# Performance work log

Hardware: AMD Instinct MI355X
Metric: run time of the kernel (lower is better)

Reference implementation:

```python
import jax, jax.numpy as jnp
import numpy as np
import math

DIM_V = 512

def setup_inputs() -> dict:
    key = jax.random.key(0)
    k1, k2, k3, k4, k5, k6 = jax.random.split(key, 6)
    B, C, N, M = 8, DIM_V, 4096, 1024
    pcd_up = jax.random.normal(k1, (B, C, N), dtype=jnp.float32)
    pcd_down = jax.random.normal(k2, (B, C, M), dtype=jnp.float32)
    s = 1.0 / math.sqrt(C)
    Wq = jax.random.normal(k3, (C, C), dtype=jnp.float32) * s
    Wk = jax.random.normal(k4, (C, C), dtype=jnp.float32) * s
    Wv = jax.random.normal(k5, (C, C), dtype=jnp.float32) * s
    Wskip = jax.random.normal(k6, (C, C), dtype=jnp.float32) * s
    return {"pcd_up": pcd_up, "pcd_down": pcd_down, "Wq": Wq, "Wk": Wk, "Wv": Wv, "Wskip": Wskip}

def reference(pcd_up, pcd_down, Wq, Wk, Wv, Wskip):
    # 1x1 Conv1d == per-point linear: weight [out_c, in_c]
    q = jnp.einsum('oc,bcn->bon', Wq, pcd_up)      # [B, C, N]
    k = jnp.einsum('oc,bcm->bom', Wk, pcd_down)    # [B, C, M]
    v = jnp.einsum('oc,bcm->bom', Wv, pcd_down)    # [B, C, M]
    C = q.shape[1]
    scale = jnp.sqrt(jnp.asarray(C, dtype=q.dtype))  # sqrt(q.shape[-2]) = sqrt(C)
    energy = jnp.einsum('bcn,bcm->bnm', q, k) / scale  # [B, N, M]
    attention = jax.nn.softmax(energy, axis=-1)
    x = jnp.einsum('bnm,bcm->bcn', attention, v)       # [B, C, N]
    skip = jnp.einsum('oc,bcn->bon', Wskip, pcd_up)
    return skip + x
```

## Files before the change

kernel.cpp:

```cpp
#include <hip/hip_runtime.h>
#include <cstddef>

#define Bn 8
#define Cd 512
#define Nn 4096
#define Mm 1024

typedef __attribute__((ext_vector_type(8))) short s8v;
typedef __attribute__((ext_vector_type(4))) float v4f;
typedef __attribute__((ext_vector_type(16))) float v16f;

__device__ __forceinline__ float b2f(unsigned short u) {
    union { unsigned int i; float f; } v; v.i = ((unsigned int)u) << 16; return v.f;
}
__device__ __forceinline__ unsigned short f2b(float f) {
    union { float f; unsigned int i; } v; v.f = f;
    unsigned int x = v.i;
    unsigned int r = (x + 0x7FFFu + ((x >> 16) & 1u)) >> 16;
    return (unsigned short)r;
}
__device__ __forceinline__ v4f mfma16(s8v a, s8v b, v4f c) {
    return __builtin_amdgcn_mfma_f32_16x16x32_bf16(a, b, c, 0, 0, 0);
}
__device__ __forceinline__ v16f mfma32(s8v a, s8v b, v16f c) {
    return __builtin_amdgcn_mfma_f32_32x32x16_bf16(a, b, c, 0, 0, 0);
}
__device__ __forceinline__ void gload_lds16(const unsigned short* gsrc, unsigned char* lds) {
    __builtin_amdgcn_global_load_lds(
        (const __attribute__((address_space(1))) unsigned int*)gsrc,
        (__attribute__((address_space(3))) unsigned int*)lds, 16, 0, 0);
}

__global__ __launch_bounds__(256) void convwf(const float* __restrict__ Wq, const float* __restrict__ Wk,
                                              const float* __restrict__ Wv, const float* __restrict__ Ws,
                                              unsigned short* __restrict__ Wf) {
    const float* S = (blockIdx.y == 0) ? Wq : (blockIdx.y == 1) ? Wk : (blockIdx.y == 2) ? Wv : Ws;
    const int o16 = blockIdx.x;
    const int t = threadIdx.x;
    const int l = t & 63, sub = t >> 6;
    const int lq = l & 15, quad = l >> 4;
    unsigned short* dst = Wf + (size_t)blockIdx.y * 262144;
#pragma unroll
    for (int rep = 0; rep < 4; ++rep) {
        int cstep = sub * 4 + rep;
        const float* src = S + (size_t)(o16 * 16 + lq) * Cd + cstep * 32 + quad * 8;
        float4 va = *(const float4*)(src);
        float4 vb = *(const float4*)(src + 4);
        union { ushort4 h[2]; uint4 q; } pk;
        pk.h[0].x = f2b(va.x); pk.h[0].y = f2b(va.y); pk.h[0].z = f2b(va.z); pk.h[0].w = f2b(va.w);
        pk.h[1].x = f2b(vb.x); pk.h[1].y = f2b(vb.y); pk.h[1].z = f2b(vb.z); pk.h[1].w = f2b(vb.w);
        *(uint4*)(dst + ((size_t)(o16 * 16 + cstep) * 64 + l) * 8) = pk.q;
    }
}

__global__ __launch_bounds__(256) void convx(const float* __restrict__ X,
                                             unsigned short* __restrict__ Xt,
                                             int Nx) {
    __shared__ float Lf[64][65];
    const int t = threadIdx.x;
    const int b = blockIdx.z, c0 = blockIdx.y * 64;
    const int nl0 = blockIdx.x * 64;
    const int cl = t >> 4, n4 = (t & 15) * 4;
    const float* Xb = X + (size_t)b * Cd * Nx + nl0;
#pragma unroll
    for (int cc = 0; cc < 4; ++cc) {
        int c = cc * 16 + cl;
        float4 v = *(const float4*)(Xb + (size_t)(c0 + c) * Nx + n4);
        Lf[n4 + 0][c] = v.x; Lf[n4 + 1][c] = v.y;
        Lf[n4 + 2][c] = v.z; Lf[n4 + 3][c] = v.w;
    }
    __syncthreads();
    unsigned short* Xtb = Xt + ((size_t)b * Nx + nl0) * Cd + c0;
#pragma unroll
    for (int rep = 0; rep < 2; ++rep) {
        int u = t + rep * 256;
        int n = u >> 3, c8 = (u & 7) * 8;
        union { ushort4 h[2]; uint4 q; } pk;
        pk.h[0].x = f2b(Lf[n][c8 + 0]); pk.h[0].y = f2b(Lf[n][c8 + 1]);
        pk.h[0].z = f2b(Lf[n][c8 + 2]); pk.h[0].w = f2b(Lf[n][c8 + 3]);
        pk.h[1].x = f2b(Lf[n][c8 + 4]); pk.h[1].y = f2b(Lf[n][c8 + 5]);
        pk.h[1].z = f2b(Lf[n][c8 + 6]); pk.h[1].w = f2b(Lf[n][c8 + 7]);
        *(uint4*)(Xtb + (size_t)n * Cd + c8) = pk.q;
    }
}

template <int PAIRB>
__global__ __launch_bounds__(256, 2) void gemm4(const unsigned short* __restrict__ Wf,
                                                unsigned short* XY,
                                                unsigned short* __restrict__ Y2,
                                                float* __restrict__ outF,
                                                int Nc) {
    __shared__ __align__(16) unsigned char raw[PAIRB ? 34816 : 8192];
    const int t = threadIdx.x;
    const int l = t & 63, w = t >> 6, lq = t & 15, quad = (t >> 4) & 3;
    const int bid = blockIdx.x;
    const int b = bid & 7, n0 = (bid >> 3) * 32;
    unsigned short* Xb = XY + ((size_t)b * Nc + n0) * Cd;
    const unsigned short* W1f = Wf + (size_t)(PAIRB ? 0 : 1) * 262144 + (size_t)l * 8;
    const unsigned short* W2f = Wf + (size_t)(PAIRB ? 3 : 2) * 262144 + (size_t)l * 8;

    v4f acc1[8][2], acc2[8][2];
#pragma unroll
    for (int i = 0; i < 8; ++i)
#pragma unroll
        for (int nt = 0; nt < 2; ++nt) {
            acc1[i][nt] = (v4f){0.f, 0.f, 0.f, 0.f};
            acc2[i][nt] = (v4f){0.f, 0.f, 0.f, 0.f};
        }

#define STAGE4(s, c0)                                                            \
    if (t < 128) gload_lds16(Xb + (size_t)(t >> 2) * Cd + (c0) + (t & 3) * 8,    \
                             raw + (s) * 2048 + t * 16);

    STAGE4(0, 0);
    for (int step = 0; step < 16; ++step) {
        const int c0 = step * 32, cur = step & 1;
        __syncthreads();
        s8v a1[8], a2[8];
#pragma unroll
        for (int i = 0; i < 8; ++i)
            a1[i] = *(const s8v*)(W1f + ((size_t)((w * 8 + i) * 16 + step) << 9));
#pragma unroll
        for (int i = 0; i < 8; ++i)
            a2[i] = *(const s8v*)(W2f + ((size_t)((w * 8 + i) * 16 + step) << 9));
        if (step < 15) { STAGE4(cur ^ 1, c0 + 32) }
        const short* Xs = (const short*)(raw + cur * 2048);
        s8v bf0 = *(const s8v*)(Xs + lq * 32 + quad * 8);
        s8v bf1 = *(const s8v*)(Xs + (lq + 16) * 32 + quad * 8);
#pragma unroll
        for (int i = 0; i < 8; ++i) {
            acc1[i][0] = mfma16(a1[i], bf0, acc1[i][0]);
            acc1[i][1] = mfma16(a1[i], bf1, acc1[i][1]);
        }
#pragma unroll
        for (int i = 0; i < 8; ++i) {
            acc2[i][0] = mfma16(a2[i], bf0, acc2[i][0]);
            acc2[i][1] = mfma16(a2[i], bf1, acc2[i][1]);
        }
    }
#undef STAGE4
    __syncthreads();

    if (PAIRB) {
#pragma unroll
        for (int i = 0; i < 8; ++i)
#pragma unroll
            for (int nt = 0; nt < 2; ++nt)
#pragma unroll
                for (int r = 0; r < 4; ++r) {
                    int o = (w * 8 + i) * 16 + quad * 4 + r;
                    int n = n0 + nt * 16 + lq;
                    outF[((size_t)b * Cd + o) * Nn + n] = acc2[i][nt][r];
                }
        short (*T2)[528] = reinterpret_cast<short(*)[528]>(raw);
#pragma unroll
        for (int i = 0; i < 8; ++i)
#pragma unroll
            for (int nt = 0; nt < 2; ++nt)
#pragma unroll
                for (int r = 0; r < 4; ++r)
                    T2[nt * 16 + lq][(w * 8 + i) * 16 + quad * 4 + r] = (short)f2b(acc1[i][nt][r]);
        __syncthreads();
        {
            int row = t >> 3, cb = (t & 7) * 64;
            unsigned short* qp = Xb + (size_t)row * Cd + cb;
#pragma unroll
            for (int j = 0; j < 8; ++j)
                *(uint4*)(qp + j * 8) = *(const uint4*)(&T2[row][cb + j * 8]);
        }
    } else {
        const int half = quad >> 1, ebase = (quad & 1) * 4;
        {
            unsigned short* Kb = XY + (size_t)b * Mm * Cd;
            const int mt = n0 >> 5;
#pragma unroll
            for (int i = 0; i < 8; ++i) {
                int kb = w * 8 + i;
#pragma unroll
                for (int nt = 0; nt < 2; ++nt) {
                    int lf = (nt * 16 + lq) + 32 * half;
                    ushort4 v;
                    v.x = f2b(acc1[i][nt][0]); v.y = f2b(acc1[i][nt][1]);
                    v.z = f2b(acc1[i][nt][2]); v.w = f2b(acc1[i][nt][3]);
                    *(ushort4*)(Kb + ((size_t)(mt * 32 + kb) * 64 + lf) * 8 + ebase) = v;
                }
            }
        }
        short (*Vst)[40] = reinterpret_cast<short(*)[40]>(raw + w * 1280);
        unsigned short* Vb0 = Y2 + (size_t)b * Cd * Mm;
#pragma unroll
        for (int i = 0; i < 8; ++i) {
#pragma unroll
            for (int nt = 0; nt < 2; ++nt)
#pragma unroll
                for (int r = 0; r < 4; ++r)
                    Vst[quad * 4 + r][nt * 16 + lq] = (short)f2b(acc2[i][nt][r]);
            int c_abs = (w * 8 + i) * 16 + (l >> 2);
            int m8 = l & 3;
            int ct = c_abs >> 5, mb = (n0 >> 4) + (m8 >> 1);
            int lf = (c_abs & 31) + 32 * (m8 & 1);
            uint4 v = *(const uint4*)(&Vst[l >> 2][m8 * 8]);
            *(uint4*)(Vb0 + ((size_t)(ct * 64 + mb) * 64 + lf) * 8) = v;
        }
    }
}

template <int MODE>
__global__ __launch_bounds__(256) void gemm_mfma(const float* __restrict__ W,
                                                 const float* __restrict__ X,
                                                 float* __restrict__ Yf,
                                                 unsigned short* __restrict__ Yb,
                                                 int Nx) {
    __shared__ short Xs[64][40];
    __shared__ short Tt[16][72];
    const int t = threadIdx.x;
    const int w = t >> 6, lq = t & 15, quad = (t >> 4) & 3;
    const int b = blockIdx.z, o0 = blockIdx.y * 64, n0 = blockIdx.x * 64;
    const float* Xb = X + (size_t)b * Cd * Nx;
    const float* Wrow = W + (size_t)(o0 + w * 16 + lq) * Cd;

    v4f acc[4];
#pragma unroll
    for (int i = 0; i < 4; ++i) acc[i] = (v4f){0.f, 0.f, 0.f, 0.f};

    for (int c0 = 0; c0 < Cd; c0 += 32) {
#pragma unroll
        for (int p = 0; p < 2; ++p) {
            int i = t + p * 256;
            int c = i >> 4;
            int n4 = (i & 15) * 4;
            float4 x = *(const float4*)(Xb + (size_t)(c0 + c) * Nx + n0 + n4);
            Xs[n4 + 0][c] = (short)f2b(x.x); Xs[n4 + 1][c] = (short)f2b(x.y);
            Xs[n4 + 2][c] = (short)f2b(x.z); Xs[n4 + 3][c] = (short)f2b(x.w);
        }
        union { unsigned short h[8]; s8v s; } af;
        {
            float4 wa = *(const float4*)(Wrow + c0 + quad * 8);
            float4 wb = *(const float4*)(Wrow + c0 + quad * 8 + 4);
            af.h[0] = f2b(wa.x); af.h[1] = f2b(wa.y); af.h[2] = f2b(wa.z); af.h[3] = f2b(wa.w);
            af.h[4] = f2b(wb.x); af.h[5] = f2b(wb.y); af.h[6] = f2b(wb.z); af.h[7] = f2b(wb.w);
        }
        __syncthreads();
#pragma unroll
        for (int nt = 0; nt < 4; ++nt) {
            s8v bf = *(const s8v*)(&Xs[nt * 16 + lq][quad * 8]);
            acc[nt] = mfma16(af.s, bf, acc[nt]);
        }
        __syncthreads();
    }

    if (MODE == 0) {
#pragma unroll
        for (int nt = 0; nt < 4; ++nt)
#pragma unroll
            for (int r = 0; r < 4; ++r) {
                int o = o0 + w * 16 + quad * 4 + r;
                int n = n0 + nt * 16 + lq;
                Yf[((size_t)b * Cd + o) * Nx + n] = acc[nt][r];
            }
    } else {
#pragma unroll
        for (int nt = 0; nt < 4; ++nt) {
#pragma unroll
            for (int r = 0; r < 4; ++r)
                Tt[lq][w * 16 + quad * 4 + r] = (short)f2b(acc[nt][r]);
            __syncthreads();
            int nrow = t >> 4, o4 = (t & 15) * 4;
            ushort4 val = *(const ushort4*)(&Tt[nrow][o4]);
            *(ushort4*)(Yb + ((size_t)b * Nx + n0 + nt * 16 + nrow) * Cd + o0 + o4) = val;
            __syncthreads();
        }
    }
}

__global__ __launch_bounds__(256, 2) void attn_v2(const unsigned short* __restrict__ Qt,
                                                  const unsigned short* __restrict__ Kf,
                                                  const unsigned short* __restrict__ Vf,
                                                  float* __restrict__ out) {
    __shared__ __align__(16) unsigned char Ls[42880];
    unsigned char* Lq = Ls;
    unsigned short* Pb = (unsigned short*)(Ls + 32768);
    float* pmaxS  = (float*)(Ls + 41472);
    float* psumS  = (float*)(Ls + 41984);
    float* muS    = (float*)(Ls + 42496);
    float* ssumS  = (float*)(Ls + 42624);
    float* alphaS = (float*)(Ls + 42752);
    float* OtA    = (float*)Ls;

    const int t = threadIdx.x;
    const int l = t & 63, w = t >> 6;
    const int lcol = l & 31, lhalf = l >> 5;
    const int bid = blockIdx.x;
    const int b = bid & 7, n0 = (bid >> 3) * 32;

    {
        const unsigned short* qb = Qt + ((size_t)b * Nn + n0) * Cd;
#pragma unroll
        for (int i = 0; i < 8; ++i) {
            int s = i * 256 + t;
            int n = s >> 6, u = s & 63;
            uint4 v = *(const uint4*)(qb + (size_t)n * Cd + u * 8);
            *(uint4*)(Lq + ((n * 64 + (u ^ (n & 15))) << 4)) = v;
        }
    }
    if (t < 32) { muS[t] = -1e30f; ssumS[t] = 0.f; }

    v16f o_acc[4];
#pragma unroll
    for (int i = 0; i < 4; ++i)
#pragma unroll
        for (int r = 0; r < 16; ++r) o_acc[i][r] = 0.f;
    __syncthreads();

    const unsigned short* Kfb = Kf + (size_t)b * Mm * Cd + (size_t)l * 8;
    const unsigned short* Vfb = Vf + (size_t)b * Cd * Mm + (size_t)l * 8;
    const int qrow = lcol * 64;
    const int swz = lcol & 15;
    const float sc = 0.04419417382415922f;

    for (int m0 = 0; m0 < Mm; m0 += 128) {
        v16f st;
#pragma unroll
        for (int r = 0; r < 16; ++r) st[r] = 0.f;
        const unsigned short* kp = Kfb + (size_t)(((m0 >> 5) + w) * 32) * 512;
#pragma unroll
        for (int kb8 = 0; kb8 < 4; ++kb8) {
            uint4 ka[8];
#pragma unroll
            for (int j = 0; j < 8; ++j) ka[j] = *(const uint4*)(kp + (size_t)(kb8 * 8 + j) * 512);
            __builtin_amdgcn_s_setprio(1);
#pragma unroll
            for (int j = 0; j < 8; ++j) {
                int kb = kb8 * 8 + j;
                s8v qf = *(const s8v*)(Lq + ((qrow + ((kb * 2 + lhalf) ^ swz)) << 4));
                union { uint4 u; s8v s; } av; av.u = ka[j];
                st = mfma32(av.s, qf, st);
            }
            __builtin_amdgcn_s_setprio(0);
        }
        uint4 v0p[8];
        {
            const unsigned short* vc = Vfb + (size_t)(w * 64 + (m0 >> 4)) * 512;
#pragma unroll
            for (int kb = 0; kb < 8; ++kb) v0p[kb] = *(const uint4*)(vc + (size_t)kb * 512);
        }
#pragma unroll
        for (int r = 0; r < 16; ++r) st[r] *= sc;
        float tm = st[0];
#pragma unroll
        for (int r = 1; r < 16; ++r) tm = fmaxf(tm, st[r]);
        tm = fmaxf(tm, __shfl_xor(tm, 32));
        if (l < 32) pmaxS[l * 4 + w] = tm;
        __syncthreads();
        if (t < 32) {
            float mx = muS[t];
            mx = fmaxf(mx, fmaxf(fmaxf(pmaxS[t * 4], pmaxS[t * 4 + 1]),
                                 fmaxf(pmaxS[t * 4 + 2], pmaxS[t * 4 + 3])));
            alphaS[t] = __expf(muS[t] - mx);
            muS[t] = mx;
        }
        __syncthreads();
        {
            float mxn = muS[lcol];
            float e[16], rs = 0.f;
#pragma unroll
            for (int r = 0; r < 16; ++r) { e[r] = __expf(st[r] - mxn); rs += e[r]; }
            rs += __shfl_xor(rs, 32);
            if (l < 32) psumS[l * 4 + w] = rs;
#pragma unroll
            for (int rg = 0; rg < 4; ++rg) {
                ushort4 pk;
                pk.x = f2b(e[rg * 4 + 0]); pk.y = f2b(e[rg * 4 + 1]);
                pk.z = f2b(e[rg * 4 + 2]); pk.w = f2b(e[rg * 4 + 3]);
                *(ushort4*)(Pb + lcol * 136 + w * 32 + 8 * rg + 4 * lhalf) = pk;
            }
        }
        __syncthreads();
        if (t < 32)
            ssumS[t] = ssumS[t] * alphaS[t] +
                       psumS[t * 4] + psumS[t * 4 + 1] + psumS[t * 4 + 2] + psumS[t * 4 + 3];

        float ar[16];
#pragma unroll
        for (int r = 0; r < 16; ++r)
            ar[r] = alphaS[(r & 3) + 8 * (r >> 2) + 4 * lhalf];
#pragma unroll
        for (int ti = 0; ti < 4; ++ti)
#pragma unroll
            for (int r = 0; r < 16; ++r) o_acc[ti][r] *= ar[r];

        s8v pA[8];
#pragma unroll
        for (int kb = 0; kb < 8; ++kb)
            pA[kb] = *(const s8v*)(Pb + lcol * 136 + kb * 16 + lhalf * 8);

#pragma unroll
        for (int ti = 0; ti < 4; ++ti) {
            uint4 vb8[8];
            if (ti == 0) {
#pragma unroll
                for (int kb = 0; kb < 8; ++kb) vb8[kb] = v0p[kb];
            } else {
                const unsigned short* vc = Vfb + (size_t)((ti * 4 + w) * 64 + (m0 >> 4)) * 512;
#pragma unroll
                for (int kb = 0; kb < 8; ++kb) vb8[kb] = *(const uint4*)(vc + (size_t)kb * 512);
            }
            __builtin_amdgcn_s_setprio(1);
#pragma unroll
            for (int kb = 0; kb < 8; ++kb) {
                union { uint4 u; s8v s; } bv; bv.u = vb8[kb];
                o_acc[ti] = mfma32(pA[kb], bv.s, o_acc[ti]);
            }
            __builtin_amdgcn_s_setprio(0);
        }
        __syncthreads();
    }

    float inv[16];
#pragma unroll
    for (int r = 0; r < 16; ++r)
        inv[r] = 1.0f / ssumS[(r & 3) + 8 * (r >> 2) + 4 * lhalf];

    float* OtW = OtA + w * 32 * 36;
#pragma unroll
    for (int ti = 0; ti < 4; ++ti) {
#pragma unroll
        for (int r = 0; r < 16; ++r)
            OtW[lcol * 36 + (r & 3) + 8 * (r >> 2) + 4 * lhalf] = o_acc[ti][r] * inv[r];
        __syncthreads();
        {
            int cloc = l >> 1, half = l & 1;
            int cabs = ti * 128 + w * 32 + cloc;
            const float* src = OtW + cloc * 36 + half * 16;
            float* op = out + ((size_t)b * Cd + cabs) * Nn + n0 + half * 16;
#pragma unroll
            for (int j = 0; j < 4; ++j) {
                float4 a = *(const float4*)(src + j * 4);
                float4 g = *(const float4*)(op + j * 4);
                g.x += a.x; g.y += a.y; g.z += a.z; g.w += a.w;
                *(float4*)(op + j * 4) = g;
            }
        }
        __syncthreads();
    }
}

__device__ __forceinline__ float u2lo(unsigned int u) {
    union { unsigned int i; float f; } v; v.i = u << 16; return v.f;
}
__device__ __forceinline__ float u2hi(unsigned int u) {
    union { unsigned int i; float f; } v; v.i = u & 0xFFFF0000u; return v.f;
}

__global__ __launch_bounds__(256) void attn_k(const float* __restrict__ up,
                                              const float* __restrict__ Wq,
                                              const unsigned short* __restrict__ Ktb,
                                              const unsigned short* __restrict__ Vtb,
                                              float* __restrict__ out) {
    __shared__ float Qs[16][516];
    __shared__ __align__(16) unsigned char Sraw[24576];
    unsigned short (*Us)[16]  = reinterpret_cast<unsigned short(*)[16]>(Sraw);
    unsigned short (*Wt)[512] = reinterpret_cast<unsigned short(*)[512]>(Sraw + 16384);
    float (*Ps)[65] = reinterpret_cast<float(*)[65]>(Sraw);
    float* mu_s     = reinterpret_cast<float*>(Sraw + 4160);
    float* ssum_s   = reinterpret_cast<float*>(Sraw + 4224);
    float* alpha_s  = reinterpret_cast<float*>(Sraw + 4288);

    const int t = threadIdx.x;
    const int b = blockIdx.y;
    const int n0 = blockIdx.x * 16;
    const int row = t & 15;
    const int grp = t >> 4;

    for (int i = t; i < Cd * 16; i += 256) {
        int c = i >> 4, r = i & 15;
        Us[c][r] = f2b(up[((size_t)b * Cd + c) * Nn + n0 + r]);
    }
    __syncthreads();

    float acc[32];
#pragma unroll
    for (int j = 0; j < 32; ++j) acc[j] = 0.f;

    for (int k0 = 0; k0 < Cd; k0 += 8) {
        for (int i = t; i < 1024; i += 256) {
            int oc = i >> 1;
            int kc = (i & 1) * 4;
            float4 wv = *(const float4*)(Wq + (size_t)oc * Cd + k0 + kc);
            Wt[kc + 0][oc] = f2b(wv.x); Wt[kc + 1][oc] = f2b(wv.y);
            Wt[kc + 2][oc] = f2b(wv.z); Wt[kc + 3][oc] = f2b(wv.w);
        }
        __syncthreads();
#pragma unroll
        for (int k = 0; k < 8; ++k) {
            float u = b2f(Us[k0 + k][row]);
            const ushort4* wr = (const ushort4*)(&Wt[k][grp * 32]);
#pragma unroll
            for (int j4 = 0; j4 < 8; ++j4) {
                ushort4 wv = wr[j4];
                acc[j4 * 4 + 0] += u * b2f(wv.x);
                acc[j4 * 4 + 1] += u * b2f(wv.y);
                acc[j4 * 4 + 2] += u * b2f(wv.z);
                acc[j4 * 4 + 3] += u * b2f(wv.w);
            }
        }
        __syncthreads();
    }

    const float scale = 0.04419417382415922f;
#pragma unroll
    for (int j = 0; j < 32; ++j) Qs[row][grp * 32 + j] = acc[j] * scale;
    if (t < 16) { mu_s[t] = -1e30f; ssum_s[t] = 0.f; }
#pragma unroll
    for (int j = 0; j < 32; ++j) acc[j] = 0.f;
    __syncthreads();

    const float4* qr = (const float4*)(&Qs[row][0]);

    for (int m0 = 0; m0 < Mm; m0 += 64) {
        {
            int mb = m0 + grp * 4;
            const uint4* K0 = (const uint4*)(Ktb + ((size_t)b * Mm + mb + 0) * Cd);
            const uint4* K1 = (const uint4*)(Ktb + ((size_t)b * Mm + mb + 1) * Cd);
            const uint4* K2 = (const uint4*)(Ktb + ((size_t)b * Mm + mb + 2) * Cd);
            const uint4* K3 = (const uint4*)(Ktb + ((size_t)b * Mm + mb + 3) * Cd);
            float a0 = 0.f, a1 = 0.f, a2 = 0.f, a3 = 0.f;
#pragma unroll 4
            for (int c8 = 0; c8 < Cd / 8; ++c8) {
                float4 qa = qr[2 * c8], qb = qr[2 * c8 + 1];
                uint4 k0v = K0[c8], k1v = K1[c8], k2v = K2[c8], k3v = K3[c8];
                a0 += qa.x * u2lo(k0v.x) + qa.y * u2hi(k0v.x) + qa.z * u2lo(k0v.y) + qa.w * u2hi(k0v.y)
                    + qb.x * u2lo(k0v.z) + qb.y * u2hi(k0v.z) + qb.z * u2lo(k0v.w) + qb.w * u2hi(k0v.w);
                a1 += qa.x * u2lo(k1v.x) + qa.y * u2hi(k1v.x) + qa.z * u2lo(k1v.y) + qa.w * u2hi(k1v.y)
                    + qb.x * u2lo(k1v.z) + qb.y * u2hi(k1v.z) + qb.z * u2lo(k1v.w) + qb.w * u2hi(k1v.w);
                a2 += qa.x * u2lo(k2v.x) + qa.y * u2hi(k2v.x) + qa.z * u2lo(k2v.y) + qa.w * u2hi(k2v.y)
                    + qb.x * u2lo(k2v.z) + qb.y * u2hi(k2v.z) + qb.z * u2lo(k2v.w) + qb.w * u2hi(k2v.w);
                a3 += qa.x * u2lo(k3v.x) + qa.y * u2hi(k3v.x) + qa.z * u2lo(k3v.y) + qa.w * u2hi(k3v.y)
                    + qb.x * u2lo(k3v.z) + qb.y * u2hi(k3v.z) + qb.z * u2lo(k3v.w) + qb.w * u2hi(k3v.w);
            }
            Ps[row][grp * 4 + 0] = a0;
            Ps[row][grp * 4 + 1] = a1;
            Ps[row][grp * 4 + 2] = a2;
            Ps[row][grp * 4 + 3] = a3;
        }
        __syncthreads();
        if (t < 16) {
            float mold = mu_s[t];
            float mx = mold;
            for (int m = 0; m < 64; ++m) mx = fmaxf(mx, Ps[t][m]);
            float al = __expf(mold - mx);
            float s = ssum_s[t] * al;
            for (int m = 0; m < 64; ++m) {
                float p = __expf(Ps[t][m] - mx);
                Ps[t][m] = p;
                s += p;
            }
            mu_s[t] = mx; ssum_s[t] = s; alpha_s[t] = al;
        }
        __syncthreads();
        {
            float arr = alpha_s[row];
#pragma unroll
            for (int j = 0; j < 32; ++j) acc[j] *= arr;
            const unsigned short* Vbase = Vtb + (size_t)b * Mm * Cd + (size_t)grp * 32;
            for (int m = 0; m < 64; ++m) {
                float p = Ps[row][m];
                const uint4* vr = (const uint4*)(Vbase + (size_t)(m0 + m) * Cd);
#pragma unroll
                for (int j4 = 0; j4 < 4; ++j4) {
                    uint4 v = vr[j4];
                    acc[j4 * 8 + 0] += p * u2lo(v.x); acc[j4 * 8 + 1] += p * u2hi(v.x);
                    acc[j4 * 8 + 2] += p * u2lo(v.y); acc[j4 * 8 + 3] += p * u2hi(v.y);
                    acc[j4 * 8 + 4] += p * u2lo(v.z); acc[j4 * 8 + 5] += p * u2hi(v.z);
                    acc[j4 * 8 + 6] += p * u2lo(v.w); acc[j4 * 8 + 7] += p * u2hi(v.w);
                }
            }
        }
        __syncthreads();
    }

    float invv = 1.0f / ssum_s[row];
#pragma unroll
    for (int j = 0; j < 32; ++j) {
        int c = grp * 32 + j;
        size_t idx = ((size_t)b * Cd + c) * Nn + n0 + row;
        out[idx] = out[idx] + acc[j] * invv;
    }
}

extern "C" void kernel_launch(void* const* d_in, const int* in_sizes, int n_in,
                              void* d_out, int out_size, void* d_ws, size_t ws_size,
                              hipStream_t stream) {
    const float* up   = (const float*)d_in[0];
    const float* down = (const float*)d_in[1];
    const float* Wq   = (const float*)d_in[2];
    const float* Wk   = (const float*)d_in[3];
    const float* Wv   = (const float*)d_in[4];
    const float* Wsk  = (const float*)d_in[5];
    float* out = (float*)d_out;

    const size_t szK = (size_t)Bn * Mm * Cd;
    const size_t szQ = (size_t)Bn * Nn * Cd;
    const size_t szW = (size_t)4 * Cd * Cd;

    if (ws_size >= (2 * szK + szQ + szW) * 2) {
        unsigned short* XK = (unsigned short*)d_ws;
        unsigned short* Vf = XK + szK;
        unsigned short* XQ = Vf + szK;
        unsigned short* Wf = XQ + szQ;
        convwf<<<dim3(32, 4), 256, 0, stream>>>(Wq, Wk, Wv, Wsk, Wf);
        convx<<<dim3(Mm / 64, Cd / 64, Bn), 256, 0, stream>>>(down, XK, Mm);
        gemm4<0><<<dim3(Bn * (Mm / 32)), 256, 0, stream>>>(Wf, XK, Vf, nullptr, Mm);
        convx<<<dim3(Nn / 64, Cd / 64, Bn), 256, 0, stream>>>(up, XQ, Nn);
        gemm4<1><<<dim3(Bn * (Nn / 32)), 256, 0, stream>>>(Wf, XQ, nullptr, out, Nn);
        attn_v2<<<dim3((Nn / 32) * Bn), 256, 0, stream>>>(XQ, XK, Vf, out);
    } else {
        unsigned short* Ktb = (unsigned short*)d_ws;
        unsigned short* Vtb = Ktb + szK;
        gemm_mfma<2><<<dim3(Mm / 64, Cd / 64, Bn), 256, 0, stream>>>(Wk, down, nullptr, Ktb, Mm);
        gemm_mfma<2><<<dim3(Mm / 64, Cd / 64, Bn), 256, 0, stream>>>(Wv, down, nullptr, Vtb, Mm);
        gemm_mfma<0><<<dim3(Nn / 64, Cd / 64, Bn), 256, 0, stream>>>(Wsk, up, out, nullptr, Nn);
        attn_k<<<dim3(Nn / 16, Bn), 256, 0, stream>>>(up, Wq, Ktb, Vtb, out);
    }
}
```

Measured before the change: 335.9 us.

## Enlarge attention tile to 64 queries and 256 keys with 512-thread blocks

Replaces attn_v2 with attn_v3, which handles 64 query rows per block using 8 waves and steps over keys in tiles of 256 instead of 128. Each K and V fragment loaded from global memory now feeds two MFMAs, one per 32-row query half, which halves K/V traffic per query row. The row max and row sum reductions are rewritten as shuffle trees over 8 partials, and the per-tile epilogue barriers are dropped because each wave uses its own staging buffer. The cost is about 104 KB of LDS per block, which likely allows only one block per CU, so latency hiding depends on the 8 waves inside that block.

```diff
diff --git a/kernel.cpp b/kernel.cpp
--- a/kernel.cpp
+++ b/kernel.cpp
@@ -273,55 +273,57 @@
     }
 }
 
-__global__ __launch_bounds__(256, 2) void attn_v2(const unsigned short* __restrict__ Qt,
+__global__ __launch_bounds__(512, 2) void attn_v3(const unsigned short* __restrict__ Qt,
                                                   const unsigned short* __restrict__ Kf,
                                                   const unsigned short* __restrict__ Vf,
                                                   float* __restrict__ out) {
-    __shared__ __align__(16) unsigned char Ls[42880];
+    __shared__ __align__(16) unsigned char Ls[104192];
     unsigned char* Lq = Ls;
-    unsigned short* Pb = (unsigned short*)(Ls + 32768);
-    float* pmaxS  = (float*)(Ls + 41472);
-    float* psumS  = (float*)(Ls + 41984);
-    float* muS    = (float*)(Ls + 42496);
-    float* ssumS  = (float*)(Ls + 42624);
-    float* alphaS = (float*)(Ls + 42752);
+    unsigned short* Pb = (unsigned short*)(Ls + 65536);
+    float* pmaxS  = (float*)(Ls + 99328);
+    float* psumS  = (float*)(Ls + 101376);
+    float* muS    = (float*)(Ls + 103424);
+    float* ssumS  = (float*)(Ls + 103680);
+    float* alphaS = (float*)(Ls + 103936);
     float* OtA    = (float*)Ls;
 
     const int t = threadIdx.x;
     const int l = t & 63, w = t >> 6;
     const int lcol = l & 31, lhalf = l >> 5;
     const int bid = blockIdx.x;
-    const int b = bid & 7, n0 = (bid >> 3) * 32;
+    const int b = bid & 7, n0 = (bid >> 3) * 64;
 
     {
         const unsigned short* qb = Qt + ((size_t)b * Nn + n0) * Cd;
 #pragma unroll
         for (int i = 0; i < 8; ++i) {
-            int s = i * 256 + t;
+            int s = i * 512 + t;
             int n = s >> 6, u = s & 63;
             uint4 v = *(const uint4*)(qb + (size_t)n * Cd + u * 8);
             *(uint4*)(Lq + ((n * 64 + (u ^ (n & 15))) << 4)) = v;
         }
     }
-    if (t < 32) { muS[t] = -1e30f; ssumS[t] = 0.f; }
-
-    v16f o_acc[4];
-#pragma unroll
-    for (int i = 0; i < 4; ++i)
-#pragma unroll
-        for (int r = 0; r < 16; ++r) o_acc[i][r] = 0.f;
+    if (t < 64) { muS[t] = -1e30f; ssumS[t] = 0.f; }
+
+    v16f o_acc[2][2];
+#pragma unroll
+    for (int nh = 0; nh < 2; ++nh)
+#pragma unroll
+        for (int ti = 0; ti < 2; ++ti)
+#pragma unroll
+            for (int r = 0; r < 16; ++r) o_acc[nh][ti][r] = 0.f;
     __syncthreads();
 
     const unsigned short* Kfb = Kf + (size_t)b * Mm * Cd + (size_t)l * 8;
     const unsigned short* Vfb = Vf + (size_t)b * Cd * Mm + (size_t)l * 8;
-    const int qrow = lcol * 64;
+    const int q0 = lcol * 64, q1 = (lcol + 32) * 64;
     const int swz = lcol & 15;
     const float sc = 0.04419417382415922f;
 
-    for (int m0 = 0; m0 < Mm; m0 += 128) {
-        v16f st;
-#pragma unroll
-        for (int r = 0; r < 16; ++r) st[r] = 0.f;
+    for (int m0 = 0; m0 < Mm; m0 += 256) {
+        v16f st0, st1;
+#pragma unroll
+        for (int r = 0; r < 16; ++r) { st0[r] = 0.f; st1[r] = 0.f; }
         const unsigned short* kp = Kfb + (size_t)(((m0 >> 5) + w) * 32) * 512;
 #pragma unroll
         for (int kb8 = 0; kb8 < 4; ++kb8) {
@@ -332,107 +334,150 @@
 #pragma unroll
             for (int j = 0; j < 8; ++j) {
                 int kb = kb8 * 8 + j;
-                s8v qf = *(const s8v*)(Lq + ((qrow + ((kb * 2 + lhalf) ^ swz)) << 4));
+                int uo = (kb * 2 + lhalf) ^ swz;
+                s8v qf0 = *(const s8v*)(Lq + ((q0 + uo) << 4));
+                s8v qf1 = *(const s8v*)(Lq + ((q1 + uo) << 4));
                 union { uint4 u; s8v s; } av; av.u = ka[j];
-                st = mfma32(av.s, qf, st);
+                st0 = mfma32(av.s, qf0, st0);
+                st1 = mfma32(av.s, qf1, st1);
             }
             __builtin_amdgcn_s_setprio(0);
         }
         uint4 v0p[8];
         {
-            const unsigned short* vc = Vfb + (size_t)(w * 64 + (m0 >> 4)) * 512;
-#pragma unroll
-            for (int kb = 0; kb < 8; ++kb) v0p[kb] = *(const uint4*)(vc + (size_t)kb * 512);
-        }
-#pragma unroll
-        for (int r = 0; r < 16; ++r) st[r] *= sc;
-        float tm = st[0];
-#pragma unroll
-        for (int r = 1; r < 16; ++r) tm = fmaxf(tm, st[r]);
-        tm = fmaxf(tm, __shfl_xor(tm, 32));
-        if (l < 32) pmaxS[l * 4 + w] = tm;
-        __syncthreads();
-        if (t < 32) {
-            float mx = muS[t];
-            mx = fmaxf(mx, fmaxf(fmaxf(pmaxS[t * 4], pmaxS[t * 4 + 1]),
-                                 fmaxf(pmaxS[t * 4 + 2], pmaxS[t * 4 + 3])));
-            alphaS[t] = __expf(muS[t] - mx);
-            muS[t] = mx;
-        }
-        __syncthreads();
-        {
-            float mxn = muS[lcol];
-            float e[16], rs = 0.f;
-#pragma unroll
-            for (int r = 0; r < 16; ++r) { e[r] = __expf(st[r] - mxn); rs += e[r]; }
-            rs += __shfl_xor(rs, 32);
-            if (l < 32) psumS[l * 4 + w] = rs;
+            const unsigned short* vc = Vfb + (size_t)((w * 2) * 64 + (m0 >> 4)) * 512;
+#pragma unroll
+            for (int j = 0; j < 8; ++j) v0p[j] = *(const uint4*)(vc + (size_t)j * 512);
+        }
+#pragma unroll
+        for (int r = 0; r < 16; ++r) { st0[r] *= sc; st1[r] *= sc; }
+        float tm0 = st0[0], tm1 = st1[0];
+#pragma unroll
+        for (int r = 1; r < 16; ++r) { tm0 = fmaxf(tm0, st0[r]); tm1 = fmaxf(tm1, st1[r]); }
+        tm0 = fmaxf(tm0, __shfl_xor(tm0, 32));
+        tm1 = fmaxf(tm1, __shfl_xor(tm1, 32));
+        if (l < 32) {
+            pmaxS[l * 8 + w] = tm0;
+            pmaxS[(l + 32) * 8 + w] = tm1;
+        }
+        __syncthreads();
+        {
+            int row = t >> 3, p = t & 7;
+            float v = pmaxS[row * 8 + p];
+            v = fmaxf(v, __shfl_xor(v, 1));
+            v = fmaxf(v, __shfl_xor(v, 2));
+            v = fmaxf(v, __shfl_xor(v, 4));
+            if (p == 0) {
+                float mold = muS[row];
+                float mx = fmaxf(mold, v);
+                alphaS[row] = __expf(mold - mx);
+                muS[row] = mx;
+            }
+        }
+        __syncthreads();
+        {
+            float mx0 = muS[lcol], mx1 = muS[lcol + 32];
+            float e0[16], e1[16], rs0 = 0.f, rs1 = 0.f;
+#pragma unroll
+            for (int r = 0; r < 16; ++r) {
+                e0[r] = __expf(st0[r] - mx0); rs0 += e0[r];
+                e1[r] = __expf(st1[r] - mx1); rs1 += e1[r];
+            }
+            rs0 += __shfl_xor(rs0, 32);
+            rs1 += __shfl_xor(rs1, 32);
+            if (l < 32) {
+                psumS[l * 8 + w] = rs0;
+                psumS[(l + 32) * 8 + w] = rs1;
+            }
 #pragma unroll
             for (int rg = 0; rg < 4; ++rg) {
-                ushort4 pk;
-                pk.x = f2b(e[rg * 4 + 0]); pk.y = f2b(e[rg * 4 + 1]);
-                pk.z = f2b(e[rg * 4 + 2]); pk.w = f2b(e[rg * 4 + 3]);
-                *(ushort4*)(Pb + lcol * 136 + w * 32 + 8 * rg + 4 * lhalf) = pk;
-            }
-        }
-        __syncthreads();
-        if (t < 32)
-            ssumS[t] = ssumS[t] * alphaS[t] +
-                       psumS[t * 4] + psumS[t * 4 + 1] + psumS[t * 4 + 2] + psumS[t * 4 + 3];
-
-        float ar[16];
-#pragma unroll
-        for (int r = 0; r < 16; ++r)
-            ar[r] = alphaS[(r & 3) + 8 * (r >> 2) + 4 * lhalf];
-#pragma unroll
-        for (int ti = 0; ti < 4; ++ti)
-#pragma unroll
-            for (int r = 0; r < 16; ++r) o_acc[ti][r] *= ar[r];
-
-        s8v pA[8];
-#pragma unroll
-        for (int kb = 0; kb < 8; ++kb)
-            pA[kb] = *(const s8v*)(Pb + lcol * 136 + kb * 16 + lhalf * 8);
-
-#pragma unroll
-        for (int ti = 0; ti < 4; ++ti) {
-            uint4 vb8[8];
-            if (ti == 0) {
-#pragma unroll
-                for (int kb = 0; kb < 8; ++kb) vb8[kb] = v0p[kb];
-            } else {
-                const unsigned short* vc = Vfb + (size_t)((ti * 4 + w) * 64 + (m0 >> 4)) * 512;
-#pragma unroll
-                for (int kb = 0; kb < 8; ++kb) vb8[kb] = *(const uint4*)(vc + (size_t)kb * 512);
-            }
-            __builtin_amdgcn_s_setprio(1);
-#pragma unroll
-            for (int kb = 0; kb < 8; ++kb) {
-                union { uint4 u; s8v s; } bv; bv.u = vb8[kb];
-                o_acc[ti] = mfma32(pA[kb], bv.s, o_acc[ti]);
-            }
-            __builtin_amdgcn_s_setprio(0);
-        }
-        __syncthreads();
-    }
-
-    float inv[16];
-#pragma unroll
-    for (int r = 0; r < 16; ++r)
-        inv[r] = 1.0f / ssumS[(r & 3) + 8 * (r >> 2) + 4 * lhalf];
-
+                ushort4 pk0, pk1;
+                pk0.x = f2b(e0[rg * 4 + 0]); pk0.y = f2b(e0[rg * 4 + 1]);
+                pk0.z = f2b(e0[rg * 4 + 2]); pk0.w = f2b(e0[rg * 4 + 3]);
+                pk1.x = f2b(e1[rg * 4 + 0]); pk1.y = f2b(e1[rg * 4 + 1]);
+                pk1.z = f2b(e1[rg * 4 + 2]); pk1.w = f2b(e1[rg * 4 + 3]);
+                *(ushort4*)(Pb + lcol * 264 + w * 32 + 8 * rg + 4 * lhalf) = pk0;
+                *(ushort4*)(Pb + (lcol + 32) * 264 + w * 32 + 8 * rg + 4 * lhalf) = pk1;
+            }
+        }
+        __syncthreads();
+        {
+            int row = t >> 3, p = t & 7;
+            float v = psumS[row * 8 + p];
+            v += __shfl_xor(v, 1);
+            v += __shfl_xor(v, 2);
+            v += __shfl_xor(v, 4);
+            if (p == 0) ssumS[row] = ssumS[row] * alphaS[row] + v;
+        }
+
+        float ar0[16], ar1[16];
+#pragma unroll
+        for (int r = 0; r < 16; ++r) {
+            int crow = (r & 3) + 8 * (r >> 2) + 4 * lhalf;
+            ar0[r] = alphaS[crow];
+            ar1[r] = alphaS[32 + crow];
+        }
+#pragma unroll
+        for (int ti = 0; ti < 2; ++ti)
+#pragma unroll
+            for (int r = 0; r < 16; ++r) {
+                o_acc[0][ti][r] *= ar0[r];
+                o_acc[1][ti][r] *= ar1[r];
+            }
+
+#pragma unroll
+        for (int h = 0; h < 2; ++h) {
+            s8v pA0[8], pA1[8];
+#pragma unroll
+            for (int j = 0; j < 8; ++j) {
+                pA0[j] = *(const s8v*)(Pb + lcol * 264 + (h * 8 + j) * 16 + lhalf * 8);
+                pA1[j] = *(const s8v*)(Pb + (lcol + 32) * 264 + (h * 8 + j) * 16 + lhalf * 8);
+            }
+#pragma unroll
+            for (int ti = 0; ti < 2; ++ti) {
+                uint4 vb[8];
+                if (h == 0 && ti == 0) {
+#pragma unroll
+                    for (int j = 0; j < 8; ++j) vb[j] = v0p[j];
+                } else {
+                    const unsigned short* vc = Vfb + (size_t)((w * 2 + ti) * 64 + (m0 >> 4) + h * 8) * 512;
+#pragma unroll
+                    for (int j = 0; j < 8; ++j) vb[j] = *(const uint4*)(vc + (size_t)j * 512);
+                }
+                __builtin_amdgcn_s_setprio(1);
+#pragma unroll
+                for (int j = 0; j < 8; ++j) {
+                    union { uint4 u; s8v s; } bv; bv.u = vb[j];
+                    o_acc[0][ti] = mfma32(pA0[j], bv.s, o_acc[0][ti]);
+                    o_acc[1][ti] = mfma32(pA1[j], bv.s, o_acc[1][ti]);
+                }
+                __builtin_amdgcn_s_setprio(0);
+            }
+        }
+        __syncthreads();
+    }
+
+    float inv0[16], inv1[16];
+#pragma unroll
+    for (int r = 0; r < 16; ++r) {
+        int crow = (r & 3) + 8 * (r >> 2) + 4 * lhalf;
+        inv0[r] = 1.0f / ssumS[crow];
+        inv1[r] = 1.0f / ssumS[32 + crow];
+    }
     float* OtW = OtA + w * 32 * 36;
 #pragma unroll
-    for (int ti = 0; ti < 4; ++ti) {
-#pragma unroll
-        for (int r = 0; r < 16; ++r)
-            OtW[lcol * 36 + (r & 3) + 8 * (r >> 2) + 4 * lhalf] = o_acc[ti][r] * inv[r];
-        __syncthreads();
-        {
+    for (int nh = 0; nh < 2; ++nh)
+#pragma unroll
+        for (int ti = 0; ti < 2; ++ti) {
+#pragma unroll
+            for (int r = 0; r < 16; ++r) {
+                int crow = (r & 3) + 8 * (r >> 2) + 4 * lhalf;
+                OtW[lcol * 36 + crow] = o_acc[nh][ti][r] * (nh ? inv1[r] : inv0[r]);
+            }
             int cloc = l >> 1, half = l & 1;
-            int cabs = ti * 128 + w * 32 + cloc;
+            int cabs = (w * 2 + ti) * 32 + cloc;
             const float* src = OtW + cloc * 36 + half * 16;
-            float* op = out + ((size_t)b * Cd + cabs) * Nn + n0 + half * 16;
+            float* op = out + ((size_t)b * Cd + cabs) * Nn + n0 + nh * 32 + half * 16;
 #pragma unroll
             for (int j = 0; j < 4; ++j) {
                 float4 a = *(const float4*)(src + j * 4);
@@ -441,8 +486,6 @@
                 *(float4*)(op + j * 4) = g;
             }
         }
-        __syncthreads();
-    }
 }
 
 __device__ __forceinline__ float u2lo(unsigned int u) {
@@ -613,7 +656,7 @@
         gemm4<0><<<dim3(Bn * (Mm / 32)), 256, 0, stream>>>(Wf, XK, Vf, nullptr, Mm);
         convx<<<dim3(Nn / 64, Cd / 64, Bn), 256, 0, stream>>>(up, XQ, Nn);
         gemm4<1><<<dim3(Bn * (Nn / 32)), 256, 0, stream>>>(Wf, XQ, nullptr, out, Nn);
-        attn_v2<<<dim3((Nn / 32) * Bn), 256, 0, stream>>>(XQ, XK, Vf, out);
+        attn_v3<<<dim3((Nn / 64) * Bn), 512, 0, stream>>>(XQ, XK, Vf, out);
     } else {
         unsigned short* Ktb = (unsigned short*)d_ws;
         unsigned short* Vtb = Ktb + szK;
```

Result: faster. 324.2 us (-3.5%).
